# Performance work log

Hardware: AMD Instinct MI355X
Metric: run time of the kernel (lower is better)

Reference implementation:

```python
import jax, jax.numpy as jnp
import numpy as np

B, T, C, H = 4, 2048, 1024, 16
D = C // H  # head dim 64


def setup_inputs() -> dict:
    key = jax.random.key(0)
    ks = jax.random.split(key, 5)
    s = 1.0 / np.sqrt(C)
    return {
        "x": jax.random.normal(ks[0], (B, T, C), jnp.float32),
        "Wq": jax.random.normal(ks[1], (C, C), jnp.float32) * s,
        "bq": jnp.zeros((C,), jnp.float32),
        "Wk": jax.random.normal(ks[2], (C, C), jnp.float32) * s,
        "bk": jnp.zeros((C,), jnp.float32),
        "Wv": jax.random.normal(ks[3], (C, C), jnp.float32) * s,
        "bv": jnp.zeros((C,), jnp.float32),
        "Wp": jax.random.normal(ks[4], (C, C), jnp.float32) * s,
        "bp": jnp.zeros((C,), jnp.float32),
    }


def reference(x, Wq, bq, Wk, bk, Wv, bv, Wp, bp):
    # project and split heads: [B,T,C] -> [B,H,T,D]
    def heads(w, b):
        return (x @ w.T + b).reshape(B, T, H, D).transpose(0, 2, 1, 3)

    q = heads(Wq, bq)
    k = heads(Wk, bk)
    v = heads(Wv, bv)

    att = jnp.einsum("bhqd,bhkd->bhqk", q, k) * (1.0 / np.sqrt(D))
    causal = jnp.tril(jnp.ones((T, T), bool))  # [T,T]
    att = jnp.where(causal[None, None], att, -jnp.inf)
    att = jax.nn.softmax(att, axis=-1)
    # dropout prob is 0.0 -> identity
    y = jnp.einsum("bhqk,bhkd->bhqd", att, v)
    y = y.transpose(0, 2, 1, 3).reshape(B, T, C)
    return y @ Wp.T + bp
```

## Files before the change

### kernel.cpp

```cpp
#include <hip/hip_runtime.h>
#include <hip/hip_bf16.h>

#define BB 4
#define TT 2048
#define CC 1024
#define HH 16
#define DD 64
#define PSTR 72

typedef unsigned short u16;
typedef __attribute__((ext_vector_type(8))) short bf16x8;
typedef __attribute__((ext_vector_type(4))) float f32x4;
typedef __attribute__((ext_vector_type(16))) float f32x16;

__device__ __forceinline__ float bf2f(u16 v) {
    union { unsigned u; float f; } c; c.u = ((unsigned)v) << 16; return c.f;
}
__device__ __forceinline__ u16 f2bf(float f) {
    union { float f; unsigned u; } c; c.f = f;
    unsigned u = c.u + 0x7fffu + ((c.u >> 16) & 1u);
    return (u16)(u >> 16);
}
__device__ __forceinline__ float fast_exp2(float x) {
    float r;
    asm volatile("v_exp_f32 %0, %1\n\ts_nop 1" : "=v"(r) : "v"(x));
    return r;
}
__device__ __forceinline__ unsigned pack_bf16(unsigned b0, unsigned b1) {
    unsigned d;
    asm("v_perm_b32 %0, %1, %2, %3" : "=v"(d) : "v"(b1), "v"(b0), "v"(0x07060302u));
    return d;
}
__device__ __forceinline__ uint2 pack4(float v0, float v1, float v2, float v3) {
    uint2 pk;
    pk.x = pack_bf16(__float_as_uint(v0) + 0x8000u, __float_as_uint(v1) + 0x8000u);
    pk.y = pack_bf16(__float_as_uint(v2) + 0x8000u, __float_as_uint(v3) + 0x8000u);
    return pk;
}
__device__ __forceinline__ void gload16(const u16* g, u16* l) {
    __builtin_amdgcn_global_load_lds(
        (const __attribute__((address_space(1))) void*)g,
        (__attribute__((address_space(3))) void*)l, 16, 0, 0);
}

__device__ __forceinline__ int detect_bf16(const u16* __restrict__ xprobe, int* sh) {
    const int t = threadIdx.x;
    u16 hh = xprobe[2 * t];
    int e = (hh >> 7) & 0xFF;
    unsigned long long m = __ballot(e >= 118 && e <= 132);
    if ((t & 63) == 0) sh[t >> 6] = __popcll(m);
    __syncthreads();
    return (sh[0] + sh[1] + sh[2] + sh[3]) >= 128;
}

struct CastArgs {
    const void* src[9];
    u16* dst[9];
    int blk_start[10];
    int n[9];
};
__global__ __launch_bounds__(256) void cast_all(CastArgs a, const u16* __restrict__ xprobe) {
    __shared__ int sh[4];
    const int isbf = detect_bf16(xprobe, sh);
    int b = blockIdx.x;
    int s = 0;
    while (s < 8 && b >= a.blk_start[s + 1]) s++;
    int i0 = (b - a.blk_start[s]) * 2048 + threadIdx.x * 8;
    if (i0 + 8 > a.n[s]) return;
    if (isbf) {
        *(uint4*)&a.dst[s][i0] = *(const uint4*)&((const u16*)a.src[s])[i0];
    } else {
        const float* sp = (const float*)a.src[s];
        u16 tmp[8];
#pragma unroll
        for (int j = 0; j < 8; j++) tmp[j] = f2bf(sp[i0 + j]);
        *(uint4*)&a.dst[s][i0] = *(uint4*)tmp;
    }
}

__device__ __forceinline__ void gemm_core(
    const u16* __restrict__ X, const u16* __restrict__ W,
    u16* Als, u16* Bls, f32x16 (&acc)[2][2],
    int m0, int n0, int wave, int lane, int wm, int wn)
{
    const int l32 = lane & 31;
    const int hv  = lane >> 5;
    int srow[4], sch[4];
#pragma unroll
    for (int c = 0; c < 4; c++) {
        srow[c] = wave * 32 + c * 8 + (lane >> 3);
        sch[c]  = (lane & 7) ^ (srow[c] & 7);
    }

    for (int k0 = 0; k0 < CC; k0 += 64) {
        __syncthreads();
#pragma unroll
        for (int c = 0; c < 4; c++) {
            gload16(&X[(size_t)(m0 + srow[c]) * CC + k0 + sch[c] * 8],
                    &Als[wave * 2048 + c * 512]);
            gload16(&W[(size_t)(n0 + srow[c]) * CC + k0 + sch[c] * 8],
                    &Bls[wave * 2048 + c * 512]);
        }
        __syncthreads();

#pragma unroll
        for (int ks = 0; ks < 4; ks++) {
            const int sw = ((ks * 2 + hv) ^ (l32 & 7)) * 8;
            bf16x8 a[2], b[2];
#pragma unroll
            for (int i = 0; i < 2; i++)
                a[i] = *(const bf16x8*)&Als[(wm + i * 32 + l32) * 64 + sw];
#pragma unroll
            for (int j = 0; j < 2; j++)
                b[j] = *(const bf16x8*)&Bls[(wn + j * 32 + l32) * 64 + sw];
#pragma unroll
            for (int i = 0; i < 2; i++)
#pragma unroll
                for (int j = 0; j < 2; j++)
                    acc[i][j] = __builtin_amdgcn_mfma_f32_32x32x16_bf16(
                        b[j], a[i], acc[i][j], 0, 0, 0);
        }
    }
}

__global__ __launch_bounds__(256, 4) void gemm_qkv(
    const u16* __restrict__ X,
    const u16* __restrict__ Wq, const u16* __restrict__ Wk, const u16* __restrict__ Wv,
    const u16* __restrict__ bq, const u16* __restrict__ bk, const u16* __restrict__ bv,
    u16* __restrict__ Q, u16* __restrict__ K, u16* __restrict__ VT)
{
    __shared__ __align__(16) u16 Als[128 * 64];
    __shared__ __align__(16) u16 Bls[128 * 64];

    const int tid  = threadIdx.x;
    const int wave = tid >> 6;
    const int lane = tid & 63;
    const int l32  = lane & 31;
    const int hv   = lane >> 5;
    const int m0   = blockIdx.x * 128;
    const int n0   = blockIdx.y * 128;
    const int z    = blockIdx.z;
    const int wm   = (wave >> 1) * 64;
    const int wn   = (wave & 1) * 64;

    const u16* W    = (z == 0) ? Wq : (z == 1) ? Wk : Wv;
    const u16* bias = (z == 0) ? bq : (z == 1) ? bk : bv;

    f32x16 acc[2][2];
#pragma unroll
    for (int i = 0; i < 2; i++)
#pragma unroll
        for (int j = 0; j < 2; j++) acc[i][j] = (f32x16)0.0f;

    gemm_core(X, W, Als, Bls, acc, m0, n0, wave, lane, wm, wn);

    const float scale = (z == 0) ? 0.18033688f : 1.0f;
    u16* outp = (z == 0) ? Q : (z == 1) ? K : VT;

#pragma unroll
    for (int j = 0; j < 2; j++) {
#pragma unroll
        for (int rq = 0; rq < 4; rq++) {
            const int n_base = n0 + wn + j * 32 + rq * 8 + hv * 4;
            union { uint2 u; u16 us[4]; } braw;
            braw.u = *(const uint2*)&bias[n_base];
            const int hh = n_base >> 6, d0 = n_base & 63;
#pragma unroll
            for (int i = 0; i < 2; i++) {
                const int m = m0 + wm + i * 32 + l32;
                const int bb = m >> 11, t = m & (TT - 1);
                float v0 = (acc[i][j][rq * 4 + 0] + bf2f(braw.us[0])) * scale;
                float v1 = (acc[i][j][rq * 4 + 1] + bf2f(braw.us[1])) * scale;
                float v2 = (acc[i][j][rq * 4 + 2] + bf2f(braw.us[2])) * scale;
                float v3 = (acc[i][j][rq * 4 + 3] + bf2f(braw.us[3])) * scale;
                if (z < 2) {
                    *(uint2*)&outp[((size_t)(bb * HH + hh) * TT + t) * DD + d0] =
                        pack4(v0, v1, v2, v3);
                } else {
                    const size_t base = (size_t)(bb * HH + hh) * DD * TT + t;
                    outp[base + (size_t)(d0 + 0) * TT] = f2bf(v0);
                    outp[base + (size_t)(d0 + 1) * TT] = f2bf(v1);
                    outp[base + (size_t)(d0 + 2) * TT] = f2bf(v2);
                    outp[base + (size_t)(d0 + 3) * TT] = f2bf(v3);
                }
            }
        }
    }
}

__global__ __launch_bounds__(256, 4) void gemm_proj(
    const u16* __restrict__ X, const u16* __restrict__ W,
    const u16* __restrict__ bias, void* __restrict__ out,
    const u16* __restrict__ xprobe)
{
    __shared__ __align__(16) u16 Als[128 * 64];
    __shared__ __align__(16) u16 Bls[128 * 64];
    __shared__ int sh[4];

    const int isbf = detect_bf16(xprobe, sh);

    const int tid  = threadIdx.x;
    const int wave = tid >> 6;
    const int lane = tid & 63;
    const int l32  = lane & 31;
    const int hv   = lane >> 5;
    const int m0   = blockIdx.x * 128;
    const int n0   = blockIdx.y * 128;
    const int wm   = (wave >> 1) * 64;
    const int wn   = (wave & 1) * 64;

    f32x16 acc[2][2];
#pragma unroll
    for (int i = 0; i < 2; i++)
#pragma unroll
        for (int j = 0; j < 2; j++) acc[i][j] = (f32x16)0.0f;

    gemm_core(X, W, Als, Bls, acc, m0, n0, wave, lane, wm, wn);

#pragma unroll
    for (int j = 0; j < 2; j++) {
#pragma unroll
        for (int rq = 0; rq < 4; rq++) {
            const int n_base = n0 + wn + j * 32 + rq * 8 + hv * 4;
            union { uint2 u; u16 us[4]; } braw;
            braw.u = *(const uint2*)&bias[n_base];
#pragma unroll
            for (int i = 0; i < 2; i++) {
                const int m = m0 + wm + i * 32 + l32;
                float v0 = acc[i][j][rq * 4 + 0] + bf2f(braw.us[0]);
                float v1 = acc[i][j][rq * 4 + 1] + bf2f(braw.us[1]);
                float v2 = acc[i][j][rq * 4 + 2] + bf2f(braw.us[2]);
                float v3 = acc[i][j][rq * 4 + 3] + bf2f(braw.us[3]);
                if (isbf) {
                    *(uint2*)&((u16*)out)[(size_t)m * CC + n_base] = pack4(v0, v1, v2, v3);
                } else {
                    float4 f; f.x = v0; f.y = v1; f.z = v2; f.w = v3;
                    *(float4*)&((float*)out)[(size_t)m * CC + n_base] = f;
                }
            }
        }
    }
}

__global__ __launch_bounds__(256, 4) void attn_kernel(
    const u16* __restrict__ Qg, const u16* __restrict__ Kg,
    const u16* __restrict__ VTg, u16* __restrict__ Yg)
{
    __shared__ __align__(16) u16 Ks[64 * 64];
    __shared__ __align__(16) u16 VTs[64 * 64];
    __shared__ __align__(16) u16 Ps[128 * PSTR];
    __shared__ float ls[128];

    const int tid  = threadIdx.x;
    const int wave = tid >> 6;
    const int lane = tid & 63;
    const int quad = lane >> 4;
    const int l16  = lane & 15;
    const int bh    = blockIdx.x;
    const int qtile = (TT / 128 - 1) - blockIdx.y;
    const int h = bh & (HH - 1);
    const int b = bh >> 4;
    const int q0 = qtile * 128;

    bf16x8 qf[2][2];
#pragma unroll
    for (int g = 0; g < 2; g++)
#pragma unroll
        for (int ks = 0; ks < 2; ks++)
            qf[g][ks] = *(const bf16x8*)&Qg[((size_t)bh * TT + q0 + wave * 32 +
                                             g * 16 + l16) * DD + ks * 32 + quad * 8];

    const int sch = (lane & 7) ^ (lane >> 3);
    const u16* kp[2];
    const u16* vp[2];
#pragma unroll
    for (int c = 0; c < 2; c++) {
        const int srow = wave * 16 + c * 8 + (lane >> 3);
        kp[c] = Kg + (size_t)bh * TT * DD + (size_t)srow * DD + sch * 8;
        vp[c] = VTg + (size_t)bh * DD * TT + (size_t)srow * TT + sch * 8;
    }

    f32x4 o_acc[2][4];
#pragma unroll
    for (int g = 0; g < 2; g++)
#pragma unroll
        for (int jt = 0; jt < 4; jt++) o_acc[g][jt] = (f32x4)0.0f;
    float lsum[2] = {0.0f, 0.0f};

    const int ntiles = 2 * qtile;

    for (int kv = 0; kv < ntiles + 2; kv++) {
        const bool masked = (kv >= ntiles);
        __syncthreads();
#pragma unroll
        for (int c = 0; c < 2; c++) {
            gload16(kp[c], &Ks[wave * 1024 + c * 512]);
            gload16(vp[c], &VTs[wave * 1024 + c * 512]);
            kp[c] += 64 * DD;
            vp[c] += 64;
        }
        __syncthreads();

        f32x4 st[2][4];
#pragma unroll
        for (int g = 0; g < 2; g++)
#pragma unroll
            for (int j = 0; j < 4; j++) st[g][j] = (f32x4)0.0f;
#pragma unroll
        for (int ks = 0; ks < 2; ks++) {
            const int rsw = ((ks * 4 + quad) ^ (l16 & 7)) * 8;
#pragma unroll
            for (int j = 0; j < 4; j++) {
                bf16x8 kf = *(const bf16x8*)&Ks[(j * 16 + l16) * 64 + rsw];
#pragma unroll
                for (int g = 0; g < 2; g++)
                    st[g][j] = __builtin_amdgcn_mfma_f32_16x16x32_bf16(
                        kf, qf[g][ks], st[g][j], 0, 0, 0);
            }
        }

#pragma unroll
        for (int g = 0; g < 2; g++) {
            u16* psrow = &Ps[(wave * 32 + g * 16 + l16) * PSTR];
            const int qrow = q0 + wave * 32 + g * 16 + l16;
            float lp = 0.0f;
#pragma unroll
            for (int j = 0; j < 4; j++) {
                float e0 = fast_exp2(st[g][j][0]);
                float e1 = fast_exp2(st[g][j][1]);
                float e2 = fast_exp2(st[g][j][2]);
                float e3 = fast_exp2(st[g][j][3]);
                if (masked) {
                    const int kc = kv * 64 + j * 16 + quad * 4;
                    if (kc + 0 > qrow) e0 = 0.0f;
                    if (kc + 1 > qrow) e1 = 0.0f;
                    if (kc + 2 > qrow) e2 = 0.0f;
                    if (kc + 3 > qrow) e3 = 0.0f;
                }
                lp += (e0 + e1) + (e2 + e3);
                uint2 pk;
                pk.x = pack_bf16(__float_as_uint(e0) + 0x8000u,
                                 __float_as_uint(e1) + 0x8000u);
                pk.y = pack_bf16(__float_as_uint(e2) + 0x8000u,
                                 __float_as_uint(e3) + 0x8000u);
                *(uint2*)&psrow[j * 16 + quad * 4] = pk;
            }
            lsum[g] += lp;
        }

#pragma unroll
        for (int ks = 0; ks < 2; ks++) {
            const int rsw = ((ks * 4 + quad) ^ (l16 & 7)) * 8;
            bf16x8 vfk[4];
#pragma unroll
            for (int jt = 0; jt < 4; jt++)
                vfk[jt] = *(const bf16x8*)&VTs[(jt * 16 + l16) * 64 + rsw];
#pragma unroll
            for (int g = 0; g < 2; g++) {
                bf16x8 pf = *(const bf16x8*)&Ps[(wave * 32 + g * 16 + l16) * PSTR +
                                                ks * 32 + quad * 8];
#pragma unroll
                for (int jt = 0; jt < 4; jt++)
                    o_acc[g][jt] = __builtin_amdgcn_mfma_f32_16x16x32_bf16(
                        pf, vfk[jt], o_acc[g][jt], 0, 0, 0);
            }
        }
    }

#pragma unroll
    for (int g = 0; g < 2; g++) {
        lsum[g] += __shfl_xor(lsum[g], 16, 64);
        lsum[g] += __shfl_xor(lsum[g], 32, 64);
        ls[wave * 32 + g * 16 + l16] = lsum[g];
    }

#pragma unroll
    for (int g = 0; g < 2; g++) {
        float linv[4];
#pragma unroll
        for (int r = 0; r < 4; r++)
            linv[r] = 1.0f / fmaxf(ls[wave * 32 + g * 16 + quad * 4 + r], 1e-20f);
#pragma unroll
        for (int jt = 0; jt < 4; jt++) {
#pragma unroll
            for (int r = 0; r < 4; r++) {
                const int t = q0 + wave * 32 + g * 16 + quad * 4 + r;
                const int c = h * DD + jt * 16 + l16;
                Yg[((size_t)b * TT + t) * CC + c] = f2bf(o_acc[g][jt][r] * linv[r]);
            }
        }
    }
}

extern "C" void kernel_launch(void* const* d_in, const int* in_sizes, int n_in,
                              void* d_out, int out_size, void* d_ws, size_t ws_size,
                              hipStream_t stream) {
    u16* w = (u16*)d_ws;
    size_t off = 0;
    const size_t NX = (size_t)BB * TT * CC;
    const size_t NW = (size_t)CC * CC;
    const size_t NB = CC;
    const size_t per = (size_t)BB * HH * TT * DD;

    u16* xb  = w + off; off += NX;
    u16* Wqb = w + off; off += NW;
    u16* Wkb = w + off; off += NW;
    u16* Wvb = w + off; off += NW;
    u16* Wpb = w + off; off += NW;
    u16* bqb = w + off; off += NB;
    u16* bkb = w + off; off += NB;
    u16* bvb = w + off; off += NB;
    u16* bpb = w + off; off += NB;
    u16* Q   = w + off; off += per;
    u16* K   = w + off; off += per;
    u16* VT  = w + off; off += per;
    u16* Y   = w + off; off += per;

    CastArgs ca;
    const int srcmap[9] = {0, 1, 3, 5, 7, 2, 4, 6, 8};
    u16* dsts[9] = {xb, Wqb, Wkb, Wvb, Wpb, bqb, bkb, bvb, bpb};
    int ns[9] = {(int)NX, (int)NW, (int)NW, (int)NW, (int)NW,
                 (int)NB, (int)NB, (int)NB, (int)NB};
    int acc_blk = 0;
    for (int i = 0; i < 9; i++) {
        ca.src[i] = d_in[srcmap[i]];
        ca.dst[i] = dsts[i];
        ca.n[i]   = ns[i];
        ca.blk_start[i] = acc_blk;
        acc_blk += (ns[i] + 2047) / 2048;
    }
    ca.blk_start[9] = acc_blk;
    cast_all<<<acc_blk, 256, 0, stream>>>(ca, (const u16*)d_in[0]);

    gemm_qkv<<<dim3(64, 8, 3), 256, 0, stream>>>(xb, Wqb, Wkb, Wvb,
                                                 bqb, bkb, bvb, Q, K, VT);
    attn_kernel<<<dim3(BB * HH, TT / 128), 256, 0, stream>>>(Q, K, VT, Y);
    gemm_proj<<<dim3(64, 8), 256, 0, stream>>>(Y, Wpb, bpb, d_out,
                                               (const u16*)d_in[0]);
}
```

Before: 255.1 us.

## Rewrite QKV and projection GEMMs as 8-wave, 4-stage pipelined kernels

Replaces the single-buffered 128x128 GEMM core with a templated 8-wave kernel that uses larger 256x256 (QKV) and 128x256 (projection) tiles. It runs a 4-deep LDS ring with K-step 32 and prefetches two tiles ahead. Global-to-LDS loads are interleaved with the MFMA phases using explicit waitcnt, barriers, sched_barrier and setprio. The goal is to hide global load latency and raise MFMA reuse per LDS byte. The cost is fewer, larger blocks with lower occupancy, more LDS, and fragile hand-tuned synchronisation.

New measurement: 309.9 us. 1.21x slower.

```diff
diff --git a/kernel.cpp b/kernel.cpp
--- a/kernel.cpp
+++ b/kernel.cpp
@@ -51,6 +51,18 @@
     if ((t & 63) == 0) sh[t >> 6] = __popcll(m);
     __syncthreads();
     return (sh[0] + sh[1] + sh[2] + sh[3]) >= 128;
+}
+__device__ __forceinline__ int detect_bf16_512(const u16* __restrict__ xprobe, int* sh) {
+    const int t = threadIdx.x;
+    u16 hh = xprobe[2 * t];
+    int e = (hh >> 7) & 0xFF;
+    unsigned long long m = __ballot(e >= 118 && e <= 132);
+    if ((t & 63) == 0) sh[t >> 6] = __popcll(m);
+    __syncthreads();
+    int s = 0;
+#pragma unroll
+    for (int w = 0; w < 8; w++) s += sh[w];
+    return s >= 256;
 }
 
 struct CastArgs {
@@ -78,95 +90,181 @@
     }
 }
 
-__device__ __forceinline__ void gemm_core(
+template<int MI>
+__device__ __forceinline__ void gemm8p(
     const u16* __restrict__ X, const u16* __restrict__ W,
-    u16* Als, u16* Bls, f32x16 (&acc)[2][2],
-    int m0, int n0, int wave, int lane, int wm, int wn)
+    u16* L, f32x16 (&acc)[MI][2],
+    int m0, int n0, int wave, int lane)
 {
+    constexpr int RA     = MI * 64;
+    constexpr int AU16   = RA * 32;
+    constexpr int BUFSTR = AU16 + 8192;
+    constexpr int NTILE  = CC / 32;
+
     const int l32 = lane & 31;
     const int hv  = lane >> 5;
-    int srow[4], sch[4];
-#pragma unroll
-    for (int c = 0; c < 4; c++) {
-        srow[c] = wave * 32 + c * 8 + (lane >> 3);
-        sch[c]  = (lane & 7) ^ (srow[c] & 7);
-    }
-
-    for (int k0 = 0; k0 < CC; k0 += 64) {
-        __syncthreads();
-#pragma unroll
-        for (int c = 0; c < 4; c++) {
-            gload16(&X[(size_t)(m0 + srow[c]) * CC + k0 + sch[c] * 8],
-                    &Als[wave * 2048 + c * 512]);
-            gload16(&W[(size_t)(n0 + srow[c]) * CC + k0 + sch[c] * 8],
-                    &Bls[wave * 2048 + c * 512]);
-        }
-        __syncthreads();
-
-#pragma unroll
-        for (int ks = 0; ks < 4; ks++) {
-            const int sw = ((ks * 2 + hv) ^ (l32 & 7)) * 8;
-            bf16x8 a[2], b[2];
-#pragma unroll
-            for (int i = 0; i < 2; i++)
-                a[i] = *(const bf16x8*)&Als[(wm + i * 32 + l32) * 64 + sw];
-#pragma unroll
-            for (int j = 0; j < 2; j++)
-                b[j] = *(const bf16x8*)&Bls[(wn + j * 32 + l32) * 64 + sw];
-#pragma unroll
-            for (int i = 0; i < 2; i++)
-#pragma unroll
-                for (int j = 0; j < 2; j++)
-                    acc[i][j] = __builtin_amdgcn_mfma_f32_32x32x16_bf16(
-                        b[j], a[i], acc[i][j], 0, 0, 0);
-        }
-    }
-}
-
-__global__ __launch_bounds__(256, 4) void gemm_qkv(
+    const int wm  = (wave >> 2) * (MI * 32);
+    const int wn  = (wave & 3) * 64;
+
+    int offA[MI][2], offB[2][2];
+#pragma unroll
+    for (int mi = 0; mi < MI; mi++)
+#pragma unroll
+        for (int ks = 0; ks < 2; ks++) {
+            const int r  = wm + mi * 32 + l32;
+            const int c  = ks * 2 + hv;
+            const int rb = r >> 3;
+            const int lo = (r & 7) ^ ((2 * c) & 7) ^ (rb & 7);
+            offA[mi][ks] = (lo + 8 * (rb + (RA / 8) * c)) * 8;
+        }
+#pragma unroll
+    for (int nj = 0; nj < 2; nj++)
+#pragma unroll
+        for (int ks = 0; ks < 2; ks++) {
+            const int r  = wn + nj * 32 + l32;
+            const int c  = ks * 2 + hv;
+            const int rb = r >> 3;
+            const int lo = (r & 7) ^ ((2 * c) & 7) ^ (rb & 7);
+            offB[nj][ks] = AU16 + (lo + 8 * (rb + 32 * c)) * 8;
+        }
+
+    const u16* pA[2];
+    int dA[2];
+#pragma unroll
+    for (int j = 0; j < MI / 2; j++) {
+        const int i  = (MI == 4) ? (wave * 128 + j * 64 + lane) : (wave * 64 + lane);
+        const int h  = i >> 3;
+        const int rb = h & (RA / 8 - 1);
+        const int c  = (MI == 4) ? (h >> 5) : (h >> 4);
+        const int r  = rb * 8 + ((lane & 7) ^ ((2 * c) & 7) ^ (rb & 7));
+        pA[j] = X + (size_t)(m0 + r) * CC + c * 8;
+        dA[j] = (i - lane) * 8;
+    }
+    const u16* pB[2];
+    int dB[2];
+#pragma unroll
+    for (int j = 0; j < 2; j++) {
+        const int i  = wave * 128 + j * 64 + lane;
+        const int h  = i >> 3;
+        const int rb = h & 31;
+        const int c  = h >> 5;
+        const int r  = rb * 8 + ((lane & 7) ^ ((2 * c) & 7) ^ (rb & 7));
+        pB[j] = W + (size_t)(n0 + r) * CC + c * 8;
+        dB[j] = AU16 + (i - lane) * 8;
+    }
+
+#pragma unroll
+    for (int pt = 0; pt < 2; pt++) {
+        u16* Lb = L + pt * BUFSTR;
+#pragma unroll
+        for (int j = 0; j < MI / 2; j++) gload16(pA[j] + pt * 32, Lb + dA[j]);
+#pragma unroll
+        for (int j = 0; j < 2; j++)      gload16(pB[j] + pt * 32, Lb + dB[j]);
+    }
+    asm volatile("s_waitcnt vmcnt(0)" ::: "memory");
+    __builtin_amdgcn_s_barrier();
+
+    bf16x8 a[MI][2], b0[2], b1[2];
+    for (int t = 0; t < NTILE; ++t) {
+        u16* Lc = L + (t & 3) * BUFSTR;
+        u16* Ln = L + ((t + 2) & 3) * BUFSTR;
+        const int kt = (t + 2 < NTILE ? t + 2 : NTILE - 1) * 32;
+
+#pragma unroll
+        for (int mi = 0; mi < MI; mi++)
+#pragma unroll
+            for (int ks = 0; ks < 2; ks++)
+                a[mi][ks] = *(const bf16x8*)&Lc[offA[mi][ks]];
+#pragma unroll
+        for (int ks = 0; ks < 2; ks++)
+            b0[ks] = *(const bf16x8*)&Lc[offB[0][ks]];
+#pragma unroll
+        for (int j = 0; j < MI / 2; j++) gload16(pA[j] + kt, Ln + dA[j]);
+        __builtin_amdgcn_sched_barrier(0);
+        if constexpr (MI == 4) asm volatile("s_waitcnt vmcnt(4)" ::: "memory");
+        else                   asm volatile("s_waitcnt vmcnt(3)" ::: "memory");
+        __builtin_amdgcn_s_barrier();
+        asm volatile("s_waitcnt lgkmcnt(0)" ::: "memory");
+        __builtin_amdgcn_sched_barrier(0);
+        __builtin_amdgcn_s_setprio(1);
+#pragma unroll
+        for (int ks = 0; ks < 2; ks++)
+#pragma unroll
+            for (int mi = 0; mi < MI; mi++)
+                acc[mi][0] = __builtin_amdgcn_mfma_f32_32x32x16_bf16(
+                    b0[ks], a[mi][ks], acc[mi][0], 0, 0, 0);
+        __builtin_amdgcn_s_setprio(0);
+        __builtin_amdgcn_sched_barrier(0);
+        __builtin_amdgcn_s_barrier();
+
+#pragma unroll
+        for (int ks = 0; ks < 2; ks++)
+            b1[ks] = *(const bf16x8*)&Lc[offB[1][ks]];
+#pragma unroll
+        for (int j = 0; j < 2; j++) gload16(pB[j] + kt, Ln + dB[j]);
+        __builtin_amdgcn_sched_barrier(0);
+        if constexpr (MI == 4) asm volatile("s_waitcnt vmcnt(4)" ::: "memory");
+        else                   asm volatile("s_waitcnt vmcnt(3)" ::: "memory");
+        __builtin_amdgcn_s_barrier();
+        asm volatile("s_waitcnt lgkmcnt(0)" ::: "memory");
+        __builtin_amdgcn_sched_barrier(0);
+        __builtin_amdgcn_s_setprio(1);
+#pragma unroll
+        for (int ks = 0; ks < 2; ks++)
+#pragma unroll
+            for (int mi = 0; mi < MI; mi++)
+                acc[mi][1] = __builtin_amdgcn_mfma_f32_32x32x16_bf16(
+                    b1[ks], a[mi][ks], acc[mi][1], 0, 0, 0);
+        __builtin_amdgcn_s_setprio(0);
+        __builtin_amdgcn_sched_barrier(0);
+        __builtin_amdgcn_s_barrier();
+    }
+}
+
+__global__ __launch_bounds__(512, 2) void gemm_qkv(
     const u16* __restrict__ X,
     const u16* __restrict__ Wq, const u16* __restrict__ Wk, const u16* __restrict__ Wv,
     const u16* __restrict__ bq, const u16* __restrict__ bk, const u16* __restrict__ bv,
     u16* __restrict__ Q, u16* __restrict__ K, u16* __restrict__ VT)
 {
-    __shared__ __align__(16) u16 Als[128 * 64];
-    __shared__ __align__(16) u16 Bls[128 * 64];
+    __shared__ __align__(16) u16 L[4 * 16384];
 
     const int tid  = threadIdx.x;
     const int wave = tid >> 6;
     const int lane = tid & 63;
     const int l32  = lane & 31;
     const int hv   = lane >> 5;
-    const int m0   = blockIdx.x * 128;
-    const int n0   = blockIdx.y * 128;
-    const int z    = blockIdx.z;
-    const int wm   = (wave >> 1) * 64;
-    const int wn   = (wave & 1) * 64;
+    const int m0   = blockIdx.x * 256;
+    const int by   = blockIdx.y;
+    const int z    = by >> 2;
+    const int n0   = (by & 3) * 256;
 
     const u16* W    = (z == 0) ? Wq : (z == 1) ? Wk : Wv;
     const u16* bias = (z == 0) ? bq : (z == 1) ? bk : bv;
 
-    f32x16 acc[2][2];
-#pragma unroll
-    for (int i = 0; i < 2; i++)
+    f32x16 acc[4][2];
+#pragma unroll
+    for (int i = 0; i < 4; i++)
 #pragma unroll
         for (int j = 0; j < 2; j++) acc[i][j] = (f32x16)0.0f;
 
-    gemm_core(X, W, Als, Bls, acc, m0, n0, wave, lane, wm, wn);
+    gemm8p<4>(X, W, &L[0], acc, m0, n0, wave, lane);
 
     const float scale = (z == 0) ? 0.18033688f : 1.0f;
     u16* outp = (z == 0) ? Q : (z == 1) ? K : VT;
+    const int wm = (wave >> 2) * 128;
+    const int wn = (wave & 3) * 64;
 
 #pragma unroll
     for (int j = 0; j < 2; j++) {
 #pragma unroll
         for (int rq = 0; rq < 4; rq++) {
-            const int n_base = n0 + wn + j * 32 + rq * 8 + hv * 4;
+            const int nn = n0 + wn + j * 32 + rq * 8 + hv * 4;
             union { uint2 u; u16 us[4]; } braw;
-            braw.u = *(const uint2*)&bias[n_base];
-            const int hh = n_base >> 6, d0 = n_base & 63;
-#pragma unroll
-            for (int i = 0; i < 2; i++) {
+            braw.u = *(const uint2*)&bias[nn];
+            const int hh = nn >> 6, d0 = nn & 63;
+#pragma unroll
+            for (int i = 0; i < 4; i++) {
                 const int m = m0 + wm + i * 32 + l32;
                 const int bb = m >> 11, t = m & (TT - 1);
                 float v0 = (acc[i][j][rq * 4 + 0] + bf2f(braw.us[0])) * scale;
@@ -188,16 +286,15 @@
     }
 }
 
-__global__ __launch_bounds__(256, 4) void gemm_proj(
+__global__ __launch_bounds__(512, 2) void gemm_proj(
     const u16* __restrict__ X, const u16* __restrict__ W,
     const u16* __restrict__ bias, void* __restrict__ out,
     const u16* __restrict__ xprobe)
 {
-    __shared__ __align__(16) u16 Als[128 * 64];
-    __shared__ __align__(16) u16 Bls[128 * 64];
-    __shared__ int sh[4];
-
-    const int isbf = detect_bf16(xprobe, sh);
+    __shared__ __align__(16) u16 L[4 * 12288];
+    __shared__ int sh[8];
+
+    const int isbf = detect_bf16_512(xprobe, sh);
 
     const int tid  = threadIdx.x;
     const int wave = tid >> 6;
@@ -205,9 +302,7 @@
     const int l32  = lane & 31;
     const int hv   = lane >> 5;
     const int m0   = blockIdx.x * 128;
-    const int n0   = blockIdx.y * 128;
-    const int wm   = (wave >> 1) * 64;
-    const int wn   = (wave & 1) * 64;
+    const int n0   = blockIdx.y * 256;
 
     f32x16 acc[2][2];
 #pragma unroll
@@ -215,15 +310,18 @@
 #pragma unroll
         for (int j = 0; j < 2; j++) acc[i][j] = (f32x16)0.0f;
 
-    gemm_core(X, W, Als, Bls, acc, m0, n0, wave, lane, wm, wn);
+    gemm8p<2>(X, W, &L[0], acc, m0, n0, wave, lane);
+
+    const int wm = (wave >> 2) * 64;
+    const int wn = (wave & 3) * 64;
 
 #pragma unroll
     for (int j = 0; j < 2; j++) {
 #pragma unroll
         for (int rq = 0; rq < 4; rq++) {
-            const int n_base = n0 + wn + j * 32 + rq * 8 + hv * 4;
+            const int nn = n0 + wn + j * 32 + rq * 8 + hv * 4;
             union { uint2 u; u16 us[4]; } braw;
-            braw.u = *(const uint2*)&bias[n_base];
+            braw.u = *(const uint2*)&bias[nn];
 #pragma unroll
             for (int i = 0; i < 2; i++) {
                 const int m = m0 + wm + i * 32 + l32;
@@ -232,10 +330,10 @@
                 float v2 = acc[i][j][rq * 4 + 2] + bf2f(braw.us[2]);
                 float v3 = acc[i][j][rq * 4 + 3] + bf2f(braw.us[3]);
                 if (isbf) {
-                    *(uint2*)&((u16*)out)[(size_t)m * CC + n_base] = pack4(v0, v1, v2, v3);
+                    *(uint2*)&((u16*)out)[(size_t)m * CC + nn] = pack4(v0, v1, v2, v3);
                 } else {
                     float4 f; f.x = v0; f.y = v1; f.z = v2; f.w = v3;
-                    *(float4*)&((float*)out)[(size_t)m * CC + n_base] = f;
+                    *(float4*)&((float*)out)[(size_t)m * CC + nn] = f;
                 }
             }
         }
@@ -432,9 +530,9 @@
     ca.blk_start[9] = acc_blk;
     cast_all<<<acc_blk, 256, 0, stream>>>(ca, (const u16*)d_in[0]);
 
-    gemm_qkv<<<dim3(64, 8, 3), 256, 0, stream>>>(xb, Wqb, Wkb, Wvb,
-                                                 bqb, bkb, bvb, Q, K, VT);
+    gemm_qkv<<<dim3(32, 12), 512, 0, stream>>>(xb, Wqb, Wkb, Wvb,
+                                               bqb, bkb, bvb, Q, K, VT);
     attn_kernel<<<dim3(BB * HH, TT / 128), 256, 0, stream>>>(Q, K, VT, Y);
-    gemm_proj<<<dim3(64, 8), 256, 0, stream>>>(Y, Wpb, bpb, d_out,
+    gemm_proj<<<dim3(64, 4), 512, 0, stream>>>(Y, Wpb, bpb, d_out,
                                                (const u16*)d_in[0]);
 }
```
